# Performance work log

Hardware: AMD Instinct MI355X
Metric: run time of the kernel (lower is better)

## Reference

```python
import jax, jax.numpy as jnp
import numpy as np

MIN_BIN_WIDTH = 1e-3
MIN_BIN_HEIGHT = 1e-3
MIN_DERIVATIVE = 1e-3
TAIL_BOUND = 10.0
EPS = 1e-6  # matches nflows searchsorted eps on the last bin edge
B, D, K = 32768, 512, 10


def setup_inputs() -> dict:
    key = jax.random.key(0)
    k1, k2, k3, k4 = jax.random.split(key, 4)
    return {
        # scale so some elements fall outside the +/- tail_bound linear tails
        "x": jax.random.normal(k1, (B, D), jnp.float32) * 4.0,
        "unnormalized_widths": jax.random.uniform(k2, (D, K), jnp.float32),
        "unnormalized_heights": jax.random.uniform(k3, (D, K), jnp.float32),
        "unnormalized_derivatives": jax.random.uniform(k4, (D, K - 1), jnp.float32),
    }


def _rqs_forward(x, uw, uh, ud):
    """Unconstrained rational-quadratic spline, forward direction.
    x: [B, D]; uw/uh: [D, K]; ud: [D, K-1]. Params shared across batch.
    Returns (y [B, D], logdet [B]).
    """
    left = -TAIL_BOUND
    right = TAIL_BOUND

    # normalized bin widths / cumulative x-knots  [D, K] / [D, K+1]
    w = jax.nn.softmax(uw, axis=-1)
    w = MIN_BIN_WIDTH + (1.0 - MIN_BIN_WIDTH * K) * w
    cw = jnp.concatenate([jnp.zeros((D, 1), w.dtype), jnp.cumsum(w, -1)], -1)
    cw = (right - left) * cw + left
    cw = cw.at[:, 0].set(left).at[:, -1].set(right)
    w = cw[:, 1:] - cw[:, :-1]

    # normalized bin heights / cumulative y-knots
    h = jax.nn.softmax(uh, axis=-1)
    h = MIN_BIN_HEIGHT + (1.0 - MIN_BIN_HEIGHT * K) * h
    ch = jnp.concatenate([jnp.zeros((D, 1), h.dtype), jnp.cumsum(h, -1)], -1)
    ch = (right - left) * ch + left
    ch = ch.at[:, 0].set(left).at[:, -1].set(right)
    h = ch[:, 1:] - ch[:, :-1]

    # boundary derivatives padded with softplus^{-1}(1 - min_derivative)
    const = np.log(np.exp(1.0 - MIN_DERIVATIVE) - 1.0).astype(np.float32)
    pad = jnp.full((D, 1), const, ud.dtype)
    d = MIN_DERIVATIVE + jax.nn.softplus(jnp.concatenate([pad, ud, pad], -1))  # [D, K+1]

    inside = (x >= left) & (x <= right)
    xc = jnp.clip(x, left, right)  # tails handled by identity below

    # per-element bin search (last edge bumped by EPS, as in nflows)
    cw_s = cw.at[:, -1].add(EPS)
    idx = jnp.sum(xc[..., None] >= cw_s[None], axis=-1) - 1  # [B, D]
    idx = jnp.clip(idx, 0, K - 1)

    feat = jnp.arange(D)[None, :]  # broadcast with idx [B, D]
    in_cw = cw[feat, idx]
    in_w = w[feat, idx]
    in_ch = ch[feat, idx]
    in_h = h[feat, idx]
    delta = h / w
    in_delta = delta[feat, idx]
    in_d = d[feat, idx]
    in_dp1 = d[feat, idx + 1]

    theta = (xc - in_cw) / in_w
    t1m = theta * (1.0 - theta)
    numerator = in_h * (in_delta * theta**2 + in_d * t1m)
    denominator = in_delta + (in_d + in_dp1 - 2.0 * in_delta) * t1m
    y = in_ch + numerator / denominator

    deriv_num = in_delta**2 * (in_dp1 * theta**2 + 2.0 * in_delta * t1m + in_d * (1.0 - theta) ** 2)
    lad = jnp.log(deriv_num) - 2.0 * jnp.log(denominator)

    y = jnp.where(inside, y, x)          # linear tails: identity
    lad = jnp.where(inside, lad, 0.0)    # logabsdet 0 in tails
    return y, jnp.sum(lad, axis=1)


def reference(x, unnormalized_widths, unnormalized_heights, unnormalized_derivatives):
    return _rqs_forward(x, unnormalized_widths, unnormalized_heights, unnormalized_derivatives)
```

## Files before the change

### kernel.cpp

```cpp
#include <hip/hip_runtime.h>

#define NB 32768
#define ND 512
#define NK 10

#define LEFTB (-10.0f)
#define RIGHTB (10.0f)
#define ROWS 8
#define NBLK 512
#define SWEEPS (NB / (NBLK * 16))

#define OFF_CWCH (9 * ND)
#define OFF_DD   (OFF_CWCH + 22 * ND)
#define OFF_PART (OFF_DD + 11 * ND)

__global__ void rqs_precompute(const float* __restrict__ uw,
                               const float* __restrict__ uh,
                               const float* __restrict__ ud,
                               float* __restrict__ ws) {
    int f = blockIdx.x * blockDim.x + threadIdx.x;
    if (f >= ND) return;

    float* E = ws;
    float2* GCWCH = (float2*)(ws + OFF_CWCH);
    float* GDD = ws + OFF_DD;

    float cw[NK + 1], ch[NK + 1], dd[NK + 1];

    {
        float u[NK];
        float m = -1e30f;
#pragma unroll
        for (int k = 0; k < NK; ++k) { u[k] = uw[f * NK + k]; m = fmaxf(m, u[k]); }
        float s = 0.0f;
#pragma unroll
        for (int k = 0; k < NK; ++k) { u[k] = expf(u[k] - m); s += u[k]; }
        float inv = 1.0f / s;
        float c = 0.0f;
        cw[0] = LEFTB;
#pragma unroll
        for (int k = 0; k < NK; ++k) {
            c += 1e-3f + (1.0f - 1e-3f * NK) * (u[k] * inv);
            cw[k + 1] = (RIGHTB - LEFTB) * c + LEFTB;
        }
        cw[NK] = RIGHTB;
    }
    {
        float u[NK];
        float m = -1e30f;
#pragma unroll
        for (int k = 0; k < NK; ++k) { u[k] = uh[f * NK + k]; m = fmaxf(m, u[k]); }
        float s = 0.0f;
#pragma unroll
        for (int k = 0; k < NK; ++k) { u[k] = expf(u[k] - m); s += u[k]; }
        float inv = 1.0f / s;
        float c = 0.0f;
        ch[0] = LEFTB;
#pragma unroll
        for (int k = 0; k < NK; ++k) {
            c += 1e-3f + (1.0f - 1e-3f * NK) * (u[k] * inv);
            ch[k + 1] = (RIGHTB - LEFTB) * c + LEFTB;
        }
        ch[NK] = RIGHTB;
    }
    dd[0] = 1.0f;
    dd[NK] = 1.0f;
#pragma unroll
    for (int k = 1; k < NK; ++k) {
        float v = ud[f * (NK - 1) + (k - 1)];
        dd[k] = 1e-3f + fmaxf(v, 0.0f) + log1pf(expf(-fabsf(v)));
    }

#pragma unroll
    for (int j = 0; j < 9; ++j) E[j * ND + f] = cw[j + 1];
#pragma unroll
    for (int k = 0; k <= NK; ++k) {
        GCWCH[k * ND + f] = make_float2(cw[k], ch[k]);
        GDD[k * ND + f] = dd[k];
    }
}

__device__ __forceinline__ float dpp_row_reduce16(float v) {
    v += __int_as_float(__builtin_amdgcn_update_dpp(
        0, __float_as_int(v), 0x111, 0xF, 0xF, true));
    v += __int_as_float(__builtin_amdgcn_update_dpp(
        0, __float_as_int(v), 0x112, 0xF, 0xF, true));
    v += __int_as_float(__builtin_amdgcn_update_dpp(
        0, __float_as_int(v), 0x114, 0xF, 0xF, true));
    v += __int_as_float(__builtin_amdgcn_update_dpp(
        0, __float_as_int(v), 0x118, 0xF, 0xF, true));
    return v;
}

__global__ __launch_bounds__(1024, 8) void rqs_main(const float* __restrict__ X,
                                                    const float* __restrict__ ws,
                                                    float* __restrict__ Y,
                                                    float* __restrict__ part) {
    const int t = threadIdx.x;
    const int fl = t & (ND - 1);
    const int hf = t >> 9;

    __shared__ float2 sCWCH[NK + 1][ND];
    __shared__ float sDD[NK + 1][ND];

    const float* E = ws;
    const float2* GCWCH = (const float2*)(ws + OFF_CWCH);
    const float* GDD = ws + OFF_DD;

    if (hf == 0) {
#pragma unroll
        for (int k = 0; k <= NK; ++k) sCWCH[k][fl] = GCWCH[k * ND + fl];
    } else {
#pragma unroll
        for (int k = 0; k <= NK; ++k) sDD[k][fl] = GDD[k * ND + fl];
    }
    float e[9];
#pragma unroll
    for (int j = 0; j < 9; ++j) e[j] = E[j * ND + fl];
    __syncthreads();

    float xs[ROWS];
    {
        const int rb = blockIdx.x * 16 + hf * ROWS;
#pragma unroll
        for (int i = 0; i < ROWS; ++i)
            xs[i] = __builtin_nontemporal_load(&X[(rb + i) * ND + fl]);
    }

    for (int it = 0; it < SWEEPS; ++it) {
        const int rb = blockIdx.x * 16 + it * (NBLK * 16) + hf * ROWS;

        float xn[ROWS];
        if (it + 1 < SWEEPS) {
            const int rn = rb + NBLK * 16;
#pragma unroll
            for (int i = 0; i < ROWS; ++i)
                xn[i] = __builtin_nontemporal_load(&X[(rn + i) * ND + fl]);
        }

        float ls[ROWS];
#pragma unroll
        for (int i = 0; i < ROWS; ++i) {
            float x = xs[i];

            int idx = 0;
#pragma unroll
            for (int j = 0; j < 9; ++j) idx += (x >= e[j]) ? 1 : 0;

            float2 c0 = sCWCH[idx][fl];
            float2 c1 = sCWCH[idx + 1][fl];
            float dk = sDD[idx][fl];
            float dk1 = sDD[idx + 1][fl];

            float w = c1.x - c0.x;
            float rw = __builtin_amdgcn_rcpf(w);
            float h = c1.y - c0.y;
            float delta = h * rw;

            float theta = (x - c0.x) * rw;
            float omt = 1.0f - theta;
            float t1m = theta * omt;
            float th2 = theta * theta;

            float num = h * fmaf(delta, th2, dk * t1m);
            float den = fmaf(fmaf(-2.0f, delta, dk + dk1), t1m, delta);
            float rden = __builtin_amdgcn_rcpf(den);
            float y = fmaf(num, rden, c0.y);

            float dnum = delta * delta *
                         (fmaf(dk1, th2, 2.0f * delta * t1m) + dk * omt * omt);
            float lad2 = __log2f(dnum * rden * rden);

            bool inside = fabsf(x) <= RIGHTB;
            __builtin_nontemporal_store(inside ? y : x, &Y[(rb + i) * ND + fl]);
            ls[i] = dpp_row_reduce16(inside ? lad2 : 0.0f);
        }

        if ((t & 15) == 15) {
            int g = fl >> 4;
#pragma unroll
            for (int i = 0; i < ROWS; ++i) part[(rb + i) * 32 + g] = ls[i];
        }

#pragma unroll
        for (int i = 0; i < ROWS; ++i) xs[i] = xn[i];
    }
}

__global__ __launch_bounds__(256) void rqs_reduce(const float* __restrict__ part,
                                                  float* __restrict__ logdet) {
    int j = blockIdx.x * 256 + threadIdx.x;
    int row = j >> 3;
    int sub = j & 7;
    float4 v = ((const float4*)part)[row * 8 + sub];
    float s = (v.x + v.y) + (v.z + v.w);
    s += __shfl_xor(s, 1, 64);
    s += __shfl_xor(s, 2, 64);
    s += __shfl_xor(s, 4, 64);
    if (sub == 0) logdet[row] = s * 0.6931471805599453f;
}

extern "C" void kernel_launch(void* const* d_in, const int* in_sizes, int n_in,
                              void* d_out, int out_size, void* d_ws, size_t ws_size,
                              hipStream_t stream) {
    const float* x  = (const float*)d_in[0];
    const float* uw = (const float*)d_in[1];
    const float* uh = (const float*)d_in[2];
    const float* ud = (const float*)d_in[3];

    float* out = (float*)d_out;
    float* Y = out;
    float* logdet = out + (size_t)NB * ND;

    float* ws = (float*)d_ws;
    float* part = ws + OFF_PART;

    hipLaunchKernelGGL(rqs_precompute, dim3(4), dim3(128), 0, stream,
                       uw, uh, ud, ws);
    hipLaunchKernelGGL(rqs_main, dim3(NBLK), dim3(1024), 0, stream,
                       x, ws, Y, part);
    hipLaunchKernelGGL(rqs_reduce, dim3(NB * 8 / 256), dim3(256), 0, stream,
                       part, logdet);
}
```

Before: 44.56 us.

## Fuse logdet reduction into main kernel via shared memory, hoist first X loads

Removes the separate reduction kernel. Each block keeps its per-row partial sums in shared memory and reduces them with shuffles after a final barrier, then writes logdet directly. This drops a kernel launch and the global round trip of the partials. The first batch of X loads is also issued before the parameter staging so it overlaps with the shared-memory fill. Y stores and the DPP reductions are grouped after the compute loop. The cost is a little more shared memory and an end-of-kernel barrier.

Result: faster. 41.22 us, median of 2 (-7.5%).

```diff
diff --git a/kernel.cpp b/kernel.cpp
--- a/kernel.cpp
+++ b/kernel.cpp
@@ -12,7 +12,6 @@
 
 #define OFF_CWCH (9 * ND)
 #define OFF_DD   (OFF_CWCH + 22 * ND)
-#define OFF_PART (OFF_DD + 11 * ND)
 
 __global__ void rqs_precompute(const float* __restrict__ uw,
                                const float* __restrict__ uh,
@@ -95,18 +94,27 @@
 __global__ __launch_bounds__(1024, 8) void rqs_main(const float* __restrict__ X,
                                                     const float* __restrict__ ws,
                                                     float* __restrict__ Y,
-                                                    float* __restrict__ part) {
+                                                    float* __restrict__ logdet) {
     const int t = threadIdx.x;
     const int fl = t & (ND - 1);
     const int hf = t >> 9;
 
     __shared__ float2 sCWCH[NK + 1][ND];
     __shared__ float sDD[NK + 1][ND];
+    __shared__ float sPart[SWEEPS * 16][32] __attribute__((aligned(16)));
 
     const float* E = ws;
     const float2* GCWCH = (const float2*)(ws + OFF_CWCH);
     const float* GDD = ws + OFF_DD;
 
+    float xs[ROWS];
+    {
+        const int rb = blockIdx.x * 16 + hf * ROWS;
+#pragma unroll
+        for (int i = 0; i < ROWS; ++i)
+            xs[i] = __builtin_nontemporal_load(&X[(rb + i) * ND + fl]);
+    }
+
     if (hf == 0) {
 #pragma unroll
         for (int k = 0; k <= NK; ++k) sCWCH[k][fl] = GCWCH[k * ND + fl];
@@ -118,14 +126,6 @@
 #pragma unroll
     for (int j = 0; j < 9; ++j) e[j] = E[j * ND + fl];
     __syncthreads();
-
-    float xs[ROWS];
-    {
-        const int rb = blockIdx.x * 16 + hf * ROWS;
-#pragma unroll
-        for (int i = 0; i < ROWS; ++i)
-            xs[i] = __builtin_nontemporal_load(&X[(rb + i) * ND + fl]);
-    }
 
     for (int it = 0; it < SWEEPS; ++it) {
         const int rb = blockIdx.x * 16 + it * (NBLK * 16) + hf * ROWS;
@@ -138,7 +138,7 @@
                 xn[i] = __builtin_nontemporal_load(&X[(rn + i) * ND + fl]);
         }
 
-        float ls[ROWS];
+        float ys[ROWS], ls[ROWS];
 #pragma unroll
         for (int i = 0; i < ROWS; ++i) {
             float x = xs[i];
@@ -172,32 +172,44 @@
             float lad2 = __log2f(dnum * rden * rden);
 
             bool inside = fabsf(x) <= RIGHTB;
-            __builtin_nontemporal_store(inside ? y : x, &Y[(rb + i) * ND + fl]);
-            ls[i] = dpp_row_reduce16(inside ? lad2 : 0.0f);
-        }
-
+            ys[i] = inside ? y : x;
+            ls[i] = inside ? lad2 : 0.0f;
+        }
+
+#pragma unroll
+        for (int i = 0; i < ROWS; ++i)
+            __builtin_nontemporal_store(ys[i], &Y[(rb + i) * ND + fl]);
+
+#pragma unroll
+        for (int i = 0; i < ROWS; ++i) ls[i] = dpp_row_reduce16(ls[i]);
         if ((t & 15) == 15) {
             int g = fl >> 4;
 #pragma unroll
-            for (int i = 0; i < ROWS; ++i) part[(rb + i) * 32 + g] = ls[i];
+            for (int i = 0; i < ROWS; ++i)
+                sPart[it * 16 + hf * ROWS + i][g] = ls[i];
         }
 
 #pragma unroll
         for (int i = 0; i < ROWS; ++i) xs[i] = xn[i];
     }
-}
-
-__global__ __launch_bounds__(256) void rqs_reduce(const float* __restrict__ part,
-                                                  float* __restrict__ logdet) {
-    int j = blockIdx.x * 256 + threadIdx.x;
-    int row = j >> 3;
-    int sub = j & 7;
-    float4 v = ((const float4*)part)[row * 8 + sub];
-    float s = (v.x + v.y) + (v.z + v.w);
-    s += __shfl_xor(s, 1, 64);
-    s += __shfl_xor(s, 2, 64);
-    s += __shfl_xor(s, 4, 64);
-    if (sub == 0) logdet[row] = s * 0.6931471805599453f;
+
+    __syncthreads();
+    {
+        const int rl = t >> 4;
+        const int c = t & 15;
+        const int it = rl >> 4;
+        const int rem = rl & 15;
+        float2 v2 = *(const float2*)&sPart[rl][c * 2];
+        float v = v2.x + v2.y;
+        v += __shfl_xor(v, 1, 16);
+        v += __shfl_xor(v, 2, 16);
+        v += __shfl_xor(v, 4, 16);
+        v += __shfl_xor(v, 8, 16);
+        if (c == 0) {
+            const int row = blockIdx.x * 16 + it * (NBLK * 16) + rem;
+            logdet[row] = v * 0.6931471805599453f;
+        }
+    }
 }
 
 extern "C" void kernel_launch(void* const* d_in, const int* in_sizes, int n_in,
@@ -213,12 +225,9 @@
     float* logdet = out + (size_t)NB * ND;
 
     float* ws = (float*)d_ws;
-    float* part = ws + OFF_PART;
 
     hipLaunchKernelGGL(rqs_precompute, dim3(4), dim3(128), 0, stream,
                        uw, uh, ud, ws);
     hipLaunchKernelGGL(rqs_main, dim3(NBLK), dim3(1024), 0, stream,
-                       x, ws, Y, part);
-    hipLaunchKernelGGL(rqs_reduce, dim3(NB * 8 / 256), dim3(256), 0, stream,
-                       part, logdet);
-}
+                       x, ws, Y, logdet);
+}
```
